# Kernel optimization log

Hardware: AMD Instinct MI355X
Metric: run time of the kernel (lower is better)

## Reference

```python
import jax, jax.numpy as jnp
import numpy as np

B, S, HID, NH, DH = 2, 1024, 4096, 32, 128
ACT_BITS, W_BITS = 8, 4
NEG_INF = float(np.finfo(np.float32).min)


def _qdq(x, bits):
    """Symmetric fake-quant over the last axis (per-token / per-out-channel), with STE."""
    qmax = 2.0 ** (bits - 1) - 1
    s = jnp.maximum(jnp.max(jnp.abs(x), axis=-1, keepdims=True) / qmax, 1e-8)
    q = jnp.clip(jnp.round(x / s), -qmax - 1, qmax) * s
    return x + jax.lax.stop_gradient(q - x)


def _rope_tables(seq_len, dim):
    inv_freq = 1.0 / (10000.0 ** (np.arange(0, dim, 2, dtype=np.float32) / dim))
    t = np.arange(seq_len, dtype=np.float32)
    freqs = np.outer(t, inv_freq)              # [S, DH/2]
    emb = np.concatenate([freqs, freqs], -1)   # [S, DH]
    return jnp.asarray(np.cos(emb)), jnp.asarray(np.sin(emb))


def _rotate_half(x):
    h = x.shape[-1] // 2
    return jnp.concatenate([-x[..., h:], x[..., :h]], axis=-1)


def _norm(x):
    return jnp.linalg.norm(x, axis=-1, keepdims=True)


def setup_inputs() -> dict:
    key = jax.random.key(0)
    ks = jax.random.split(key, 5)
    causal = jnp.where(jnp.tril(jnp.ones((S, S), dtype=bool)), 0.0, NEG_INF).astype(jnp.float32)
    return {
        "hidden_states": jax.random.normal(ks[0], (B, S, HID), jnp.float32),
        "wq": jax.random.normal(ks[1], (HID, HID), jnp.float32) * 0.02,
        "wk": jax.random.normal(ks[2], (HID, HID), jnp.float32) * 0.02,
        "wv": jax.random.normal(ks[3], (HID, HID), jnp.float32) * 0.02,
        "wo": jax.random.normal(ks[4], (HID, HID), jnp.float32) * 0.02,
        "attention_mask": jnp.broadcast_to(causal[None, None], (B, 1, S, S)),
    }


def reference(hidden_states, wq, wk, wv, wo, attention_mask):
    cos, sin = _rope_tables(S, DH)
    cos, sin = cos[None, None], sin[None, None]          # [1,1,S,DH]
    x = _qdq(hidden_states, ACT_BITS)                    # act fake-quant (per token)

    def proj(w):
        return jnp.einsum('bsh,dh->bsd', x, _qdq(w, W_BITS)).reshape(B, S, NH, DH).transpose(0, 2, 1, 3)

    q, k, v = proj(wq), proj(wk), proj(wv)               # [B,H,S,D]
    q = q * cos + _rotate_half(q) * sin
    k = k * cos + _rotate_half(k) * sin

    # qkt_matmul: quant Q and K, rescale scores by quantization norm ratios a1, a2
    x1len = _norm(q)
    qq = _qdq(q, ACT_BITS)
    a1 = _norm(qq) / x1len                               # [B,H,S,1]
    x2len = _norm(k)
    kq = _qdq(k, ACT_BITS)
    a2 = jnp.swapaxes(_norm(kq) / x2len, 2, 3)           # [B,H,1,S]

    attn = jnp.einsum('bhqd,bhkd->bhqk', qq, kq) / np.float32(np.sqrt(DH))
    attn = attn / a1 / a2
    attn = attn + attention_mask
    attn = jnp.maximum(attn, NEG_INF)
    p = jax.nn.softmax(attn.astype(jnp.float32), axis=-1)

    # pv_matmul: quant P and V, rescale output by V's norm ratio
    pq = _qdq(p, ACT_BITS)
    x2len_v = _norm(v)
    vq = _qdq(v, ACT_BITS)
    a2v = _norm(vq) / x2len_v                            # [B,H,S,1]

    out = jnp.einsum('bhqk,bhkd->bhqd', pq, vq) / a2v    # [B,H,S,D]
    out = out.transpose(0, 2, 1, 3).reshape(B, S, HID)
    out = jnp.einsum('bsh,dh->bsd', _qdq(out, ACT_BITS), _qdq(wo, W_BITS))
    return out
```

## Files before the change

kernel.cpp:

```cpp
#include <hip/hip_runtime.h>
#include <hip/hip_bf16.h>
#include <math.h>
#include <stdint.h>

#define NEG_INF_F (-3.4028234663852886e38f)

typedef __bf16 bf16_t;
typedef __bf16 bf16x8 __attribute__((ext_vector_type(8)));
typedef float f32x4 __attribute__((ext_vector_type(4)));
typedef float f32x16 __attribute__((ext_vector_type(16)));
typedef int i32x4 __attribute__((ext_vector_type(4)));
typedef int i32x16 __attribute__((ext_vector_type(16)));
typedef int8_t c8x4 __attribute__((ext_vector_type(4)));

static constexpr int Bb = 2, Ss = 1024, Hid = 4096, Nh = 32, Dh = 128;
static constexpr int Mr = Bb * Ss;
static constexpr int Bh = Bb * Nh;

__device__ __forceinline__ void gload_lds16(const void* g, void* l) {
  __builtin_amdgcn_global_load_lds((const __attribute__((address_space(1))) void*)g,
                                   (__attribute__((address_space(3))) void*)l, 16, 0, 0);
}

__device__ __forceinline__ float wred_max(float v) {
#pragma unroll
  for (int off = 32; off > 0; off >>= 1) v = fmaxf(v, __shfl_xor(v, off));
  return v;
}

__device__ __forceinline__ unsigned pkbf(float a, float b) {
  unsigned short ua = __builtin_bit_cast(unsigned short, (bf16_t)a);
  unsigned short ub = __builtin_bit_cast(unsigned short, (bf16_t)b);
  return (unsigned)ua | ((unsigned)ub << 16);
}

__global__ void rope_table_kernel(float* __restrict__ ctab, float* __restrict__ stab) {
  int i = blockIdx.x * 256 + threadIdx.x;
  int srow = i >> 6, d = i & 63;
  float invf = (float)pow(10000.0, -((double)(2 * d) / (double)Dh));
  float ang = (float)srow * invf;
  ctab[i] = (float)cos((double)ang);
  stab[i] = (float)sin((double)ang);
}

__device__ __forceinline__ void quant_row_body(
    const float* __restrict__ x, int8_t* __restrict__ o, float* __restrict__ scale,
    int row, int ncols, float qmax, float clo, float chi)
{
  const int tid = threadIdx.x;
  const float4* x4 = (const float4*)x;
  const int n4 = ncols >> 2;
  float m = 0.f;
  for (int i = tid; i < n4; i += 256) {
    float4 v = x4[i];
    m = fmaxf(m, fmaxf(fmaxf(fabsf(v.x), fabsf(v.y)), fmaxf(fabsf(v.z), fabsf(v.w))));
  }
  m = wred_max(m);
  __shared__ float red[4];
  if ((tid & 63) == 0) red[tid >> 6] = m;
  __syncthreads();
  m = fmaxf(fmaxf(red[0], red[1]), fmaxf(red[2], red[3]));
  const float s = fmaxf(m / qmax, 1e-8f);
  if (tid == 0) scale[row] = s;
  c8x4* o4 = (c8x4*)o;
  for (int i = tid; i < n4; i += 256) {
    float4 v = x4[i];
    c8x4 r;
    r[0] = (int8_t)(int)fminf(fmaxf(rintf(v.x / s), clo), chi);
    r[1] = (int8_t)(int)fminf(fmaxf(rintf(v.y / s), clo), chi);
    r[2] = (int8_t)(int)fminf(fmaxf(rintf(v.z / s), clo), chi);
    r[3] = (int8_t)(int)fminf(fmaxf(rintf(v.w / s), clo), chi);
    o4[i] = r;
  }
}

__global__ __launch_bounds__(256) void quant_rows_kernel(
    const float* __restrict__ in, int8_t* __restrict__ outq,
    float* __restrict__ scale, int ncols, float qmax, float clo, float chi)
{
  const int row = blockIdx.x;
  quant_row_body(in + (size_t)row * ncols, outq + (size_t)row * ncols, scale,
                 row, ncols, qmax, clo, chi);
}

__global__ __launch_bounds__(256) void quant_w4_kernel(
    const float* __restrict__ w0, const float* __restrict__ w1,
    const float* __restrict__ w2, const float* __restrict__ w3,
    int8_t* __restrict__ o0, int8_t* __restrict__ o1,
    int8_t* __restrict__ o2, int8_t* __restrict__ o3,
    float* __restrict__ s0, float* __restrict__ s1,
    float* __restrict__ s2, float* __restrict__ s3)
{
  const int sel = blockIdx.x >> 12, row = blockIdx.x & 4095;
  const float* in = sel == 0 ? w0 : (sel == 1 ? w1 : (sel == 2 ? w2 : w3));
  int8_t* o = sel == 0 ? o0 : (sel == 1 ? o1 : (sel == 2 ? o2 : o3));
  float* sc = sel == 0 ? s0 : (sel == 1 ? s1 : (sel == 2 ? s2 : s3));
  quant_row_body(in + (size_t)row * Hid, o + (size_t)row * Hid, sc, row, Hid,
                 7.f, -8.f, 7.f);
}

#define GEMM_WAITBAR(N)                                                               \
  asm volatile("s_waitcnt vmcnt(" #N ")" ::: "memory");                               \
  __builtin_amdgcn_sched_barrier(0);                                                  \
  __builtin_amdgcn_s_barrier();                                                       \
  __builtin_amdgcn_sched_barrier(0);

#define GEMM_BARONLY                                                                  \
  __builtin_amdgcn_sched_barrier(0);                                                  \
  __builtin_amdgcn_s_barrier();                                                       \
  __builtin_amdgcn_sched_barrier(0);

#define GEMM_STAGE128(koff, Abuf, Bbuf)                                               \
  _Pragma("unroll")                                                                   \
  for (int r = 0; r < 4; ++r) {                                                       \
    gload_lds16(gA + (koff) + (size_t)r * 32 * K, (Abuf) + r * 4096 + wid * 1024);    \
    gload_lds16(gB + (koff) + (size_t)r * 32 * K, (Bbuf) + r * 4096 + wid * 1024);    \
  }

#define GEMM_PHASE128(Abuf, Bbuf)                                                     \
  _Pragma("unroll")                                                                   \
  for (int g = 0; g < 2; ++g) {                                                       \
    i32x4 af[4], bw[4];                                                               \
    _Pragma("unroll")                                                                 \
    for (int f = 0; f < 4; ++f) {                                                     \
      const int ca = (((g << 2) | kg4) ^ (l15 & 7)) * 16;                             \
      af[f] = *(const i32x4*)&(Abuf)[(wm * 64 + f * 16 + l15) * 128 + ca];            \
      bw[f] = *(const i32x4*)&(Bbuf)[(f * 32 + wn * 16 + l15) * 128 + ca];            \
    }                                                                                 \
    _Pragma("unroll")                                                                 \
    for (int fm = 0; fm < 4; ++fm)                                                    \
      _Pragma("unroll")                                                               \
      for (int fn = 0; fn < 4; ++fn)                                                  \
        acc[fm][fn] = __builtin_amdgcn_mfma_i32_16x16x64_i8(af[fm], bw[fn],           \
                                                            acc[fm][fn], 0, 0, 0);   \
  }

#define GEMM_CORE_PIPE(SMEM)                                                          \
  int8_t* A0 = (int8_t*)(SMEM);                                                       \
  int8_t* A1 = (int8_t*)(SMEM) + 16384;                                               \
  int8_t* B0 = (int8_t*)(SMEM) + 32768;                                               \
  int8_t* B1 = (int8_t*)(SMEM) + 49152;                                               \
  const int strow = wid * 8 + (lane >> 3);                                            \
  const int schunk = ((lane & 7) ^ (lane >> 3)) * 16;                                 \
  const int8_t* gA = A + (size_t)(bm + strow) * K + schunk;                           \
  const int8_t* gB = W + (size_t)(bn + strow) * K + schunk;                           \
  i32x4 acc[4][4] = {};                                                               \
  GEMM_STAGE128(0, A0, B0)                                                            \
  GEMM_STAGE128(128, A1, B1)                                                          \
  for (int k0 = 0; k0 + 512 <= K; k0 += 256) {                                        \
    GEMM_WAITBAR(8)                                                                   \
    GEMM_PHASE128(A0, B0)                                                             \
    GEMM_BARONLY                                                                      \
    GEMM_STAGE128(k0 + 256, A0, B0)                                                   \
    GEMM_WAITBAR(8)                                                                   \
    GEMM_PHASE128(A1, B1)                                                             \
    GEMM_BARONLY                                                                      \
    GEMM_STAGE128(k0 + 384, A1, B1)                                                   \
  }                                                                                   \
  GEMM_WAITBAR(8)                                                                     \
  GEMM_PHASE128(A0, B0)                                                               \
  GEMM_BARONLY                                                                        \
  GEMM_WAITBAR(0)                                                                     \
  GEMM_PHASE128(A1, B1)

__global__ __launch_bounds__(256) void qkv_gemm_kernel(
    const int8_t* __restrict__ A, const float* __restrict__ sA,
    const int8_t* __restrict__ wqz, const int8_t* __restrict__ wkz, const int8_t* __restrict__ wvz,
    const float* __restrict__ swq, const float* __restrict__ swk, const float* __restrict__ swv,
    int8_t* __restrict__ qqb, float* __restrict__ Fq,
    int8_t* __restrict__ kqb, float* __restrict__ Fk,
    bf16_t* __restrict__ vdq, float* __restrict__ a2vp,
    const float* __restrict__ ctab, const float* __restrict__ stab)
{
  __shared__ __align__(16) char smem[65536 + 3072];
  float (*s_red)[128][3] = (float (*)[128][3])(smem + 65536);

  const int tid = threadIdx.x, lane = tid & 63, wid = tid >> 6;
  const int id = blockIdx.x;
  const int xcd = id & 7, within = id >> 3;
  const int nIdx = xcd * 12 + (within >> 4);
  const int mIdx = within & 15;
  const int wsel = nIdx >> 5, head = nIdx & 31;
  const int bm = mIdx * 128, bn = head * 128;
  const int8_t* W = wsel == 0 ? wqz : (wsel == 1 ? wkz : wvz);
  const float* sW = wsel == 0 ? swq : (wsel == 1 ? swk : swv);
  constexpr int K = Hid;

  const int wm = wid >> 1, wn = wid & 1;
  const int l15 = lane & 15, kg4 = lane >> 4;

  GEMM_CORE_PIPE(smem)

  float sav[4][4], swv_[4];
#pragma unroll
  for (int fm = 0; fm < 4; ++fm)
#pragma unroll
    for (int j = 0; j < 4; ++j) sav[fm][j] = sA[bm + wm * 64 + fm * 16 + kg4 * 4 + j];
#pragma unroll
  for (int fn = 0; fn < 4; ++fn) swv_[fn] = sW[bn + fn * 32 + wn * 16 + l15];

  float val[4][4][4];
#pragma unroll
  for (int fm = 0; fm < 4; ++fm)
#pragma unroll
    for (int fn = 0; fn < 4; ++fn)
#pragma unroll
      for (int j = 0; j < 4; ++j)
        val[fm][fn][j] = (float)acc[fm][fn][j] * sav[fm][j] * swv_[fn];

  const int b = bm >> 10;
  const int bh = b * Nh + head;
  float r_[4][4][4];
  if (wsel != 2) {
    const int dmA = wn * 16 + l15, dmB = 32 + wn * 16 + l15;
#pragma unroll
    for (int fm = 0; fm < 4; ++fm)
#pragma unroll
      for (int j = 0; j < 4; ++j) {
        const int srow = (bm + wm * 64 + fm * 16 + kg4 * 4 + j) & (Ss - 1);
        const float cA = ctab[srow * 64 + dmA], cB = ctab[srow * 64 + dmB];
        const float sA_ = stab[srow * 64 + dmA], sB_ = stab[srow * 64 + dmB];
        r_[fm][0][j] = __fsub_rn(__fmul_rn(val[fm][0][j], cA), __fmul_rn(val[fm][2][j], sA_));
        r_[fm][1][j] = __fsub_rn(__fmul_rn(val[fm][1][j], cB), __fmul_rn(val[fm][3][j], sB_));
        r_[fm][2][j] = __fadd_rn(__fmul_rn(val[fm][2][j], cA), __fmul_rn(val[fm][0][j], sA_));
        r_[fm][3][j] = __fadd_rn(__fmul_rn(val[fm][3][j], cB), __fmul_rn(val[fm][1][j], sB_));
      }
  } else {
#pragma unroll
    for (int fm = 0; fm < 4; ++fm)
#pragma unroll
      for (int fn = 0; fn < 4; ++fn)
#pragma unroll
        for (int j = 0; j < 4; ++j) r_[fm][fn][j] = val[fm][fn][j];
  }
  float ma_[4][4], n2_[4][4];
#pragma unroll
  for (int fm = 0; fm < 4; ++fm)
#pragma unroll
    for (int j = 0; j < 4; ++j) {
      float ma = 0.f, n2 = 0.f;
#pragma unroll
      for (int fn = 0; fn < 4; ++fn) {
        const float x = r_[fm][fn][j];
        ma = fmaxf(ma, fabsf(x));
        n2 += x * x;
      }
#pragma unroll
      for (int off = 1; off < 16; off <<= 1) {
        ma = fmaxf(ma, __shfl_xor(ma, off));
        n2 += __shfl_xor(n2, off);
      }
      ma_[fm][j] = ma;
      n2_[fm][j] = n2;
    }
  if (l15 == 0) {
#pragma unroll
    for (int fm = 0; fm < 4; ++fm)
#pragma unroll
      for (int j = 0; j < 4; ++j) {
        const int rl = wm * 64 + fm * 16 + kg4 * 4 + j;
        s_red[wn][rl][0] = ma_[fm][j];
        s_red[wn][rl][1] = n2_[fm][j];
      }
  }
  __syncthreads();
  float qc[4][4][4], svl[4][4], n2c[4][4], nq2_[4][4];
#pragma unroll
  for (int fm = 0; fm < 4; ++fm)
#pragma unroll
    for (int j = 0; j < 4; ++j) {
      const int rl = wm * 64 + fm * 16 + kg4 * 4 + j;
      const float ma = fmaxf(ma_[fm][j], s_red[wn ^ 1][rl][0]);
      const float n2 = n2_[fm][j] + s_red[wn ^ 1][rl][1];
      const float s = fmaxf(ma / 127.0f, 1e-8f);
      float nq2 = 0.f;
#pragma unroll
      for (int fn = 0; fn < 4; ++fn) {
        const float q = fminf(fmaxf(rintf(r_[fm][fn][j] / s), -128.f), 127.f);
        qc[fm][fn][j] = q;
        nq2 += q * q;
      }
#pragma unroll
      for (int off = 1; off < 16; off <<= 1) nq2 += __shfl_xor(nq2, off);
      svl[fm][j] = s;
      n2c[fm][j] = n2;
      nq2_[fm][j] = nq2;
    }
  __syncthreads();
  if (l15 == 0) {
#pragma unroll
    for (int fm = 0; fm < 4; ++fm)
#pragma unroll
      for (int j = 0; j < 4; ++j)
        s_red[wn][wm * 64 + fm * 16 + kg4 * 4 + j][2] = nq2_[fm][j];
  }
  __syncthreads();

  if (wsel != 2) {
    int8_t* outq = (wsel == 0) ? qqb : kqb;
    float* Ff = (wsel == 0) ? Fq : Fk;
#pragma unroll
    for (int fm = 0; fm < 4; ++fm)
#pragma unroll
      for (int j = 0; j < 4; ++j) {
        const int rl = wm * 64 + fm * 16 + kg4 * 4 + j;
        const int stok = (bm + rl) & (Ss - 1);
        const size_t rowBase = ((size_t)bh * Ss + stok) * Dh;
#pragma unroll
        for (int fn = 0; fn < 4; ++fn)
          outq[rowBase + fn * 32 + wn * 16 + l15] = (int8_t)(int)qc[fm][fn][j];
        if (wn == 0 && l15 == 0) {
          const float nq2 = nq2_[fm][j] + s_red[1][rl][2];
          Ff[(size_t)bh * Ss + stok] = sqrtf(n2c[fm][j] / nq2) * 0.2973017787506803f;
        }
      }
  } else {
    bf16_t* svt = (bf16_t*)smem;
#pragma unroll
    for (int fm = 0; fm < 4; ++fm)
#pragma unroll
      for (int j = 0; j < 4; ++j) {
        const int t = wm * 64 + fm * 16 + kg4 * 4 + j;
#pragma unroll
        for (int fn = 0; fn < 4; ++fn) {
          const int d = fn * 32 + wn * 16 + l15;
          svt[d * 136 + t] = (bf16_t)(qc[fm][fn][j] * svl[fm][j]);
        }
        if (wn == 0 && l15 == 0) {
          const float nq2 = nq2_[fm][j] + s_red[1][t][2];
          a2vp[(size_t)bh * Ss + ((bm + t) & (Ss - 1))] =
              svl[fm][j] * sqrtf(nq2) / sqrtf(n2c[fm][j]);
        }
      }
    __syncthreads();
    const int d = tid >> 1, toff = (tid & 1) * 64;
    const int s0 = bm & (Ss - 1);
    const bf16_t* src = svt + d * 136 + toff;
    bf16_t* dst = vdq + ((size_t)bh * Dh + d) * Ss + s0 + toff;
#pragma unroll
    for (int k = 0; k < 8; ++k) {
      bf16x8 tv;
#pragma unroll
      for (int e = 0; e < 8; ++e) tv[e] = src[k * 8 + e];
      *(bf16x8*)(dst + k * 8) = tv;
    }
  }
}

__global__ __launch_bounds__(256) void gemm0_kernel(
    const int8_t* __restrict__ A, const float* __restrict__ sA,
    const int8_t* __restrict__ W, const float* __restrict__ sW,
    float* __restrict__ out, int M, int N, int K)
{
  __shared__ __align__(16) int8_t As[128 * 128];
  __shared__ __align__(16) int8_t Bs[128 * 128];
  const int tid = threadIdx.x, lane = tid & 63, wid = tid >> 6;
  const int id = blockIdx.x;
  const int xcd = id & 7, within = id >> 3;
  const int nIdx = xcd * 4 + (within >> 4);
  const int mIdx = within & 15;
  const int bm = mIdx * 128, bn = nIdx * 128;
  const int wm = wid >> 1, wn = wid & 1;
  const int l15 = lane & 15, kg4 = lane >> 4;

  const int strow = wid * 8 + (lane >> 3);
  const int schunk = ((lane & 7) ^ (lane >> 3)) * 16;
  const int8_t* gA = A + (size_t)(bm + strow) * K + schunk;
  const int8_t* gB = W + (size_t)(bn + strow) * K + schunk;

  i32x4 acc[4][4] = {};
  for (int k0 = 0; k0 < K; k0 += 128) {
    if (k0) __syncthreads();
#pragma unroll
    for (int r = 0; r < 4; ++r) {
      gload_lds16(gA + k0 + (size_t)r * 32 * K, As + r * 4096 + wid * 1024);
      gload_lds16(gB + k0 + (size_t)r * 32 * K, Bs + r * 4096 + wid * 1024);
    }
    __syncthreads();
#pragma unroll
    for (int g = 0; g < 2; ++g) {
      i32x4 af[4], bw[4];
#pragma unroll
      for (int f = 0; f < 4; ++f) {
        const int ca = (((g << 2) | kg4) ^ (l15 & 7)) * 16;
        af[f] = *(const i32x4*)&As[(wm * 64 + f * 16 + l15) * 128 + ca];
        bw[f] = *(const i32x4*)&Bs[(f * 32 + wn * 16 + l15) * 128 + ca];
      }
#pragma unroll
      for (int fm = 0; fm < 4; ++fm)
#pragma unroll
        for (int fn = 0; fn < 4; ++fn)
          acc[fm][fn] = __builtin_amdgcn_mfma_i32_16x16x64_i8(af[fm], bw[fn], acc[fm][fn], 0, 0, 0);
    }
  }
#pragma unroll
  for (int fm = 0; fm < 4; ++fm) {
#pragma unroll
    for (int j = 0; j < 4; ++j) {
      const int row = bm + wm * 64 + fm * 16 + kg4 * 4 + j;
      const float sa = sA[row];
#pragma unroll
      for (int fn = 0; fn < 4; ++fn) {
        const int col = bn + fn * 32 + wn * 16 + l15;
        out[(size_t)row * N + col] = (float)acc[fm][fn][j] * sa * sW[col];
      }
    }
  }
}

#define KR(r) (((r) & 3) + 8 * ((r) >> 2) + 4 * hi)
__global__ __launch_bounds__(64, 2) void attn_kernel(
    const int8_t* __restrict__ qq, const int8_t* __restrict__ kq,
    const bf16_t* __restrict__ vdqt,
    const float* __restrict__ Fq, const float* __restrict__ Fk,
    const float* __restrict__ A2v, float* __restrict__ oattn)
{
  const int bh = blockIdx.x, b = bh >> 5, h = bh & 31;
  const int lane = threadIdx.x & 63;
  const int l31 = lane & 31, hi = lane >> 5;
  const int u = 31 - (int)blockIdx.y;
  const int q0 = u * 32;
  const int nt = u + 1;
  const size_t bhS = (size_t)bh * Ss;

  const int8_t* qrow = qq + (bhS + q0 + l31) * Dh + hi * 16;
  i32x4 qf[4];
#pragma unroll
  for (int c = 0; c < 4; ++c) qf[c] = *(const i32x4*)(qrow + c * 32);
  const float fq = Fq[bhS + q0 + l31];
  const int qcol = q0 + l31;

  float m = NEG_INF_F;
  int t = 0;
  for (; t + 1 < nt; t += 2) {
    const int kb0 = t * 32, kb1 = kb0 + 32;
    const int8_t* kr0 = kq + (bhS + kb0 + l31) * Dh + hi * 16;
    const int8_t* kr1 = kq + (bhS + kb1 + l31) * Dh + hi * 16;
    i32x16 ca = {}, cb = {}, da = {}, db = {};
    ca = __builtin_amdgcn_mfma_i32_32x32x32_i8(*(const i32x4*)(kr0),      qf[0], ca, 0, 0, 0);
    cb = __builtin_amdgcn_mfma_i32_32x32x32_i8(*(const i32x4*)(kr0 + 64), qf[2], cb, 0, 0, 0);
    da = __builtin_amdgcn_mfma_i32_32x32x32_i8(*(const i32x4*)(kr1),      qf[0], da, 0, 0, 0);
    db = __builtin_amdgcn_mfma_i32_32x32x32_i8(*(const i32x4*)(kr1 + 64), qf[2], db, 0, 0, 0);
    ca = __builtin_amdgcn_mfma_i32_32x32x32_i8(*(const i32x4*)(kr0 + 32), qf[1], ca, 0, 0, 0);
    cb = __builtin_amdgcn_mfma_i32_32x32x32_i8(*(const i32x4*)(kr0 + 96), qf[3], cb, 0, 0, 0);
    da = __builtin_amdgcn_mfma_i32_32x32x32_i8(*(const i32x4*)(kr1 + 32), qf[1], da, 0, 0, 0);
    db = __builtin_amdgcn_mfma_i32_32x32x32_i8(*(const i32x4*)(kr1 + 96), qf[3], db, 0, 0, 0);
    float4 fk40[4], fk41[4];
#pragma unroll
    for (int g = 0; g < 4; ++g) fk40[g] = *(const float4*)&Fk[bhS + kb0 + g * 8 + 4 * hi];
#pragma unroll
    for (int g = 0; g < 4; ++g) fk41[g] = *(const float4*)&Fk[bhS + kb1 + g * 8 + 4 * hi];
    const bool diag1 = (t + 1 == nt - 1);
#pragma unroll
    for (int r = 0; r < 16; ++r) {
      m = fmaxf(m, (float)(ca[r] + cb[r]) * fq * ((const float*)&fk40[r >> 2])[r & 3]);
      const float v1 = (float)(da[r] + db[r]) * fq * ((const float*)&fk41[r >> 2])[r & 3];
      if (!diag1 || (kb1 + KR(r) <= qcol)) m = fmaxf(m, v1);
    }
  }
  if (t < nt) {
    const int kb = t * 32;
    const int8_t* krow = kq + (bhS + kb + l31) * Dh + hi * 16;
    i32x16 ca = {}, cb = {};
    ca = __builtin_amdgcn_mfma_i32_32x32x32_i8(*(const i32x4*)(krow),      qf[0], ca, 0, 0, 0);
    cb = __builtin_amdgcn_mfma_i32_32x32x32_i8(*(const i32x4*)(krow + 64), qf[2], cb, 0, 0, 0);
    ca = __builtin_amdgcn_mfma_i32_32x32x32_i8(*(const i32x4*)(krow + 32), qf[1], ca, 0, 0, 0);
    cb = __builtin_amdgcn_mfma_i32_32x32x32_i8(*(const i32x4*)(krow + 96), qf[3], cb, 0, 0, 0);
    float4 fk4[4];
#pragma unroll
    for (int g = 0; g < 4; ++g) fk4[g] = *(const float4*)&Fk[bhS + kb + g * 8 + 4 * hi];
#pragma unroll
    for (int r = 0; r < 16; ++r) {
      const float v = (float)(ca[r] + cb[r]) * fq * ((const float*)&fk4[r >> 2])[r & 3];
      if (kb + KR(r) <= qcol) m = fmaxf(m, v);
    }
  }
  m = fmaxf(m, __shfl_xor(m, 32));

  float z = 0.f;
  f32x16 oacc[4] = {};
  for (int tt = 0; tt < nt; ++tt) {
    const int kb = tt * 32;
    const int8_t* krow = kq + (bhS + kb + l31) * Dh + hi * 16;
    i32x16 ca = {}, cb = {};
    ca = __builtin_amdgcn_mfma_i32_32x32x32_i8(*(const i32x4*)(krow),      qf[0], ca, 0, 0, 0);
    cb = __builtin_amdgcn_mfma_i32_32x32x32_i8(*(const i32x4*)(krow + 64), qf[2], cb, 0, 0, 0);
    ca = __builtin_amdgcn_mfma_i32_32x32x32_i8(*(const i32x4*)(krow + 32), qf[1], ca, 0, 0, 0);
    cb = __builtin_amdgcn_mfma_i32_32x32x32_i8(*(const i32x4*)(krow + 96), qf[3], cb, 0, 0, 0);
    float4 fk4[4];
#pragma unroll
    for (int g = 0; g < 4; ++g) fk4[g] = *(const float4*)&Fk[bhS + kb + g * 8 + 4 * hi];
    float p[16];
    const bool diag = (tt == nt - 1);
#pragma unroll
    for (int r = 0; r < 16; ++r) {
      float v = (float)(ca[r] + cb[r]) * fq * ((const float*)&fk4[r >> 2])[r & 3];
      if (diag && (kb + KR(r) > qcol)) v = NEG_INF_F;
      const float e = __expf(v - m);
      z += e;
      p[r] = rintf(127.0f * e);
    }
#pragma unroll
    for (int s = 0; s < 2; ++s) {
      const int rs = s * 8;
      unsigned k0 = pkbf(p[rs + 0], p[rs + 1]);
      unsigned k1 = pkbf(p[rs + 2], p[rs + 3]);
      unsigned k2 = pkbf(p[rs + 4], p[rs + 5]);
      unsigned k3 = pkbf(p[rs + 6], p[rs + 7]);
      unsigned sx0 = __shfl_xor(k0, 32);
      unsigned sx1 = __shfl_xor(k1, 32);
      unsigned sx2 = __shfl_xor(k2, 32);
      unsigned sx3 = __shfl_xor(k3, 32);
      uint4 ww;
      ww.x = hi ? sx2 : k0;
      ww.y = hi ? sx3 : k1;
      ww.z = hi ? k2 : sx0;
      ww.w = hi ? k3 : sx1;
      const bf16x8 af = __builtin_bit_cast(bf16x8, ww);
      const int kg2 = kb + s * 16 + hi * 8;
#pragma unroll
      for (int dt = 0; dt < 4; ++dt) {
        const bf16x8 vf = *(const bf16x8*)(vdqt + ((size_t)bh * Dh + dt * 32 + l31) * Ss + kg2);
        oacc[dt] = __builtin_amdgcn_mfma_f32_32x32x16_bf16(af, vf, oacc[dt], 0, 0, 0);
      }
    }
  }
  z += __shfl_xor(z, 32);
  const float osc = (1.0f / z) / 127.0f / A2v[bhS + q0 + l31];
#pragma unroll
  for (int dt = 0; dt < 4; ++dt) {
#pragma unroll
    for (int r = 0; r < 16; ++r) {
      const int q = q0 + KR(r);
      const float oscr = __shfl(osc, KR(r));
      oattn[((size_t)b * Ss + q) * Hid + h * Dh + dt * 32 + l31] = oacc[dt][r] * oscr;
    }
  }
}

extern "C" void kernel_launch(void* const* d_in, const int* in_sizes, int n_in,
                              void* d_out, int out_size, void* d_ws, size_t ws_size,
                              hipStream_t stream)
{
  const float* hidden = (const float*)d_in[0];
  const float* wq = (const float*)d_in[1];
  const float* wk = (const float*)d_in[2];
  const float* wv = (const float*)d_in[3];
  const float* wo = (const float*)d_in[4];
  float* out = (float*)d_out;

  char* p = (char*)d_ws;
  auto alloc = [&](size_t bytes) -> char* {
    char* r = p; p += (bytes + 255) & ~(size_t)255; return r;
  };
  int8_t* xq   = (int8_t*)alloc((size_t)Mr * Hid);
  int8_t* wb0  = (int8_t*)alloc((size_t)Hid * Hid);
  int8_t* wb1  = (int8_t*)alloc((size_t)Hid * Hid);
  int8_t* wb2  = (int8_t*)alloc((size_t)Hid * Hid);
  int8_t* wb3  = (int8_t*)alloc((size_t)Hid * Hid);
  float*  oat  = (float*) alloc((size_t)Bh * Ss * Dh * sizeof(float));
  int8_t* qqb  = (int8_t*)alloc((size_t)Bh * Ss * Dh);
  int8_t* kqb  = (int8_t*)alloc((size_t)Bh * Ss * Dh);
  bf16_t* vdqt = (bf16_t*)alloc((size_t)Bh * Dh * Ss * sizeof(bf16_t));
  float* sxa = (float*)alloc((size_t)Mr * sizeof(float));
  float* sw0 = (float*)alloc((size_t)Hid * sizeof(float));
  float* sw1 = (float*)alloc((size_t)Hid * sizeof(float));
  float* sw2 = (float*)alloc((size_t)Hid * sizeof(float));
  float* sw3 = (float*)alloc((size_t)Hid * sizeof(float));
  float* Fq  = (float*)alloc((size_t)Bh * Ss * sizeof(float));
  float* Fk  = (float*)alloc((size_t)Bh * Ss * sizeof(float));
  float* A2v = (float*)alloc((size_t)Bh * Ss * sizeof(float));
  float* soa = (float*)alloc((size_t)Mr * sizeof(float));
  float* ctab = (float*)alloc((size_t)Ss * 64 * sizeof(float));
  float* stab = (float*)alloc((size_t)Ss * 64 * sizeof(float));
  int8_t* oq  = xq;

  rope_table_kernel<<<Ss * 64 / 256, 256, 0, stream>>>(ctab, stab);
  quant_rows_kernel<<<Mr, 256, 0, stream>>>(hidden, xq, sxa, Hid, 127.f, -128.f, 127.f);
  quant_w4_kernel<<<4 * Hid, 256, 0, stream>>>(wq, wk, wv, wo, wb0, wb1, wb2, wb3,
                                               sw0, sw1, sw2, sw3);

  qkv_gemm_kernel<<<1536, 256, 0, stream>>>(xq, sxa, wb0, wb1, wb2, sw0, sw1, sw2,
                                            qqb, Fq, kqb, Fk, vdqt, A2v, ctab, stab);

  dim3 ga(Bh, 32);
  attn_kernel<<<ga, 64, 0, stream>>>(qqb, kqb, vdqt, Fq, Fk, A2v, oat);

  quant_rows_kernel<<<Mr, 256, 0, stream>>>(oat, oq, soa, Hid, 127.f, -128.f, 127.f);
  gemm0_kernel<<<512, 256, 0, stream>>>(oq, soa, wb3, sw3, out, Mr, Hid, Hid);
}
```

Before: 373.1 us.

## Enlarge QKV GEMM tile to 256x128 with 64-wide K stages

The fused QKV int8 GEMM now computes 256x128 output tiles per block (8x4 MFMA fragments per wave) using K-steps of 64 instead of 128, halving the grid to 768 blocks. Each B fragment is reused across more A rows, which cuts global and LDS traffic per MFMA and shrinks the shared-memory footprint to 48KB by reusing staging buffers for the reduction and transpose scratch. The epilogue is reworked to store V's transposed tile in two halves and to reuse one register array in place. The trade is higher register pressure (128 accumulator registers), which may lower occupancy, plus fewer blocks to spread across the CUs.

```diff
diff --git a/kernel.cpp b/kernel.cpp
--- a/kernel.cpp
+++ b/kernel.cpp
@@ -99,69 +99,40 @@
                  7.f, -8.f, 7.f);
 }
 
-#define GEMM_WAITBAR(N)                                                               \
+#define QKV_WAITBAR(N)                                                                \
   asm volatile("s_waitcnt vmcnt(" #N ")" ::: "memory");                               \
   __builtin_amdgcn_sched_barrier(0);                                                  \
   __builtin_amdgcn_s_barrier();                                                       \
   __builtin_amdgcn_sched_barrier(0);
 
-#define GEMM_BARONLY                                                                  \
+#define QKV_BARONLY                                                                   \
   __builtin_amdgcn_sched_barrier(0);                                                  \
   __builtin_amdgcn_s_barrier();                                                       \
   __builtin_amdgcn_sched_barrier(0);
 
-#define GEMM_STAGE128(koff, Abuf, Bbuf)                                               \
+#define QKV_STAGE(koff, Abuf, Bbuf)                                                   \
   _Pragma("unroll")                                                                   \
-  for (int r = 0; r < 4; ++r) {                                                       \
-    gload_lds16(gA + (koff) + (size_t)r * 32 * K, (Abuf) + r * 4096 + wid * 1024);    \
-    gload_lds16(gB + (koff) + (size_t)r * 32 * K, (Bbuf) + r * 4096 + wid * 1024);    \
-  }
-
-#define GEMM_PHASE128(Abuf, Bbuf)                                                     \
+  for (int r = 0; r < 4; ++r)                                                         \
+    gload_lds16(gA + (koff) + (size_t)r * 64 * K, (Abuf) + r * 4096 + wid * 1024);    \
   _Pragma("unroll")                                                                   \
-  for (int g = 0; g < 2; ++g) {                                                       \
-    i32x4 af[4], bw[4];                                                               \
+  for (int r = 0; r < 2; ++r)                                                         \
+    gload_lds16(gB + (koff) + (size_t)r * 64 * K, (Bbuf) + r * 4096 + wid * 1024);
+
+#define QKV_PHASE(Abuf, Bbuf)                                                         \
+  {                                                                                   \
+    i32x4 bw[4];                                                                      \
     _Pragma("unroll")                                                                 \
-    for (int f = 0; f < 4; ++f) {                                                     \
-      const int ca = (((g << 2) | kg4) ^ (l15 & 7)) * 16;                             \
-      af[f] = *(const i32x4*)&(Abuf)[(wm * 64 + f * 16 + l15) * 128 + ca];            \
-      bw[f] = *(const i32x4*)&(Bbuf)[(f * 32 + wn * 16 + l15) * 128 + ca];            \
-    }                                                                                 \
+    for (int f = 0; f < 4; ++f)                                                       \
+      bw[f] = *(const i32x4*)&(Bbuf)[(f * 32 + wn * 16 + l15) * 64 + ck];             \
     _Pragma("unroll")                                                                 \
-    for (int fm = 0; fm < 4; ++fm)                                                    \
+    for (int fm = 0; fm < 8; ++fm) {                                                  \
+      i32x4 af = *(const i32x4*)&(Abuf)[(wm * 128 + fm * 16 + l15) * 64 + ck];        \
       _Pragma("unroll")                                                               \
       for (int fn = 0; fn < 4; ++fn)                                                  \
-        acc[fm][fn] = __builtin_amdgcn_mfma_i32_16x16x64_i8(af[fm], bw[fn],           \
+        acc[fm][fn] = __builtin_amdgcn_mfma_i32_16x16x64_i8(af, bw[fn],               \
                                                             acc[fm][fn], 0, 0, 0);   \
-  }
-
-#define GEMM_CORE_PIPE(SMEM)                                                          \
-  int8_t* A0 = (int8_t*)(SMEM);                                                       \
-  int8_t* A1 = (int8_t*)(SMEM) + 16384;                                               \
-  int8_t* B0 = (int8_t*)(SMEM) + 32768;                                               \
-  int8_t* B1 = (int8_t*)(SMEM) + 49152;                                               \
-  const int strow = wid * 8 + (lane >> 3);                                            \
-  const int schunk = ((lane & 7) ^ (lane >> 3)) * 16;                                 \
-  const int8_t* gA = A + (size_t)(bm + strow) * K + schunk;                           \
-  const int8_t* gB = W + (size_t)(bn + strow) * K + schunk;                           \
-  i32x4 acc[4][4] = {};                                                               \
-  GEMM_STAGE128(0, A0, B0)                                                            \
-  GEMM_STAGE128(128, A1, B1)                                                          \
-  for (int k0 = 0; k0 + 512 <= K; k0 += 256) {                                        \
-    GEMM_WAITBAR(8)                                                                   \
-    GEMM_PHASE128(A0, B0)                                                             \
-    GEMM_BARONLY                                                                      \
-    GEMM_STAGE128(k0 + 256, A0, B0)                                                   \
-    GEMM_WAITBAR(8)                                                                   \
-    GEMM_PHASE128(A1, B1)                                                             \
-    GEMM_BARONLY                                                                      \
-    GEMM_STAGE128(k0 + 384, A1, B1)                                                   \
-  }                                                                                   \
-  GEMM_WAITBAR(8)                                                                     \
-  GEMM_PHASE128(A0, B0)                                                               \
-  GEMM_BARONLY                                                                        \
-  GEMM_WAITBAR(0)                                                                     \
-  GEMM_PHASE128(A1, B1)
+    }                                                                                 \
+  }
 
 __global__ __launch_bounds__(256) void qkv_gemm_kernel(
     const int8_t* __restrict__ A, const float* __restrict__ sA,
@@ -172,76 +143,98 @@
     bf16_t* __restrict__ vdq, float* __restrict__ a2vp,
     const float* __restrict__ ctab, const float* __restrict__ stab)
 {
-  __shared__ __align__(16) char smem[65536 + 3072];
-  float (*s_red)[128][3] = (float (*)[128][3])(smem + 65536);
+  __shared__ __align__(16) char smem[49152];
+  int8_t* A0 = (int8_t*)smem;
+  int8_t* B0 = (int8_t*)smem + 16384;
+  int8_t* A1 = (int8_t*)smem + 24576;
+  int8_t* B1 = (int8_t*)smem + 40960;
+  float (*s_red)[256][3] = (float (*)[256][3])smem;
+  bf16_t* svt = (bf16_t*)(smem + 8192);
 
   const int tid = threadIdx.x, lane = tid & 63, wid = tid >> 6;
   const int id = blockIdx.x;
   const int xcd = id & 7, within = id >> 3;
-  const int nIdx = xcd * 12 + (within >> 4);
-  const int mIdx = within & 15;
+  const int nIdx = xcd * 12 + (within >> 3);
+  const int mIdx = within & 7;
   const int wsel = nIdx >> 5, head = nIdx & 31;
-  const int bm = mIdx * 128, bn = head * 128;
+  const int bm = mIdx * 256, bn = head * 128;
   const int8_t* W = wsel == 0 ? wqz : (wsel == 1 ? wkz : wvz);
   const float* sW = wsel == 0 ? swq : (wsel == 1 ? swk : swv);
   constexpr int K = Hid;
 
   const int wm = wid >> 1, wn = wid & 1;
   const int l15 = lane & 15, kg4 = lane >> 4;
-
-  GEMM_CORE_PIPE(smem)
-
-  float sav[4][4], swv_[4];
-#pragma unroll
-  for (int fm = 0; fm < 4; ++fm)
-#pragma unroll
-    for (int j = 0; j < 4; ++j) sav[fm][j] = sA[bm + wm * 64 + fm * 16 + kg4 * 4 + j];
+  const int ck = (kg4 ^ ((l15 >> 1) & 3)) * 16;
+
+  const int strow = tid >> 2;
+  const int schunk = ((tid & 3) ^ ((tid >> 3) & 3)) * 16;
+  const int8_t* gA = A + (size_t)(bm + strow) * K + schunk;
+  const int8_t* gB = W + (size_t)(bn + strow) * K + schunk;
+
+  i32x4 acc[8][4] = {};
+  QKV_STAGE(0, A0, B0)
+  QKV_STAGE(64, A1, B1)
+  for (int k0 = 0; k0 + 256 <= K; k0 += 128) {
+    QKV_WAITBAR(6)
+    QKV_PHASE(A0, B0)
+    QKV_BARONLY
+    QKV_STAGE(k0 + 128, A0, B0)
+    QKV_WAITBAR(6)
+    QKV_PHASE(A1, B1)
+    QKV_BARONLY
+    QKV_STAGE(k0 + 192, A1, B1)
+  }
+  QKV_WAITBAR(6)
+  QKV_PHASE(A0, B0)
+  QKV_BARONLY
+  QKV_WAITBAR(0)
+  QKV_PHASE(A1, B1)
+
+  float sav[8][4], swv_[4];
+#pragma unroll
+  for (int fm = 0; fm < 8; ++fm)
+#pragma unroll
+    for (int j = 0; j < 4; ++j) sav[fm][j] = sA[bm + wm * 128 + fm * 16 + kg4 * 4 + j];
 #pragma unroll
   for (int fn = 0; fn < 4; ++fn) swv_[fn] = sW[bn + fn * 32 + wn * 16 + l15];
 
-  float val[4][4][4];
-#pragma unroll
-  for (int fm = 0; fm < 4; ++fm)
+  float w[8][4][4];
+#pragma unroll
+  for (int fm = 0; fm < 8; ++fm)
 #pragma unroll
     for (int fn = 0; fn < 4; ++fn)
 #pragma unroll
       for (int j = 0; j < 4; ++j)
-        val[fm][fn][j] = (float)acc[fm][fn][j] * sav[fm][j] * swv_[fn];
+        w[fm][fn][j] = (float)acc[fm][fn][j] * sav[fm][j] * swv_[fn];
 
   const int b = bm >> 10;
   const int bh = b * Nh + head;
-  float r_[4][4][4];
   if (wsel != 2) {
     const int dmA = wn * 16 + l15, dmB = 32 + wn * 16 + l15;
 #pragma unroll
-    for (int fm = 0; fm < 4; ++fm)
+    for (int fm = 0; fm < 8; ++fm)
 #pragma unroll
       for (int j = 0; j < 4; ++j) {
-        const int srow = (bm + wm * 64 + fm * 16 + kg4 * 4 + j) & (Ss - 1);
+        const int srow = (bm + wm * 128 + fm * 16 + kg4 * 4 + j) & (Ss - 1);
         const float cA = ctab[srow * 64 + dmA], cB = ctab[srow * 64 + dmB];
         const float sA_ = stab[srow * 64 + dmA], sB_ = stab[srow * 64 + dmB];
-        r_[fm][0][j] = __fsub_rn(__fmul_rn(val[fm][0][j], cA), __fmul_rn(val[fm][2][j], sA_));
-        r_[fm][1][j] = __fsub_rn(__fmul_rn(val[fm][1][j], cB), __fmul_rn(val[fm][3][j], sB_));
-        r_[fm][2][j] = __fadd_rn(__fmul_rn(val[fm][2][j], cA), __fmul_rn(val[fm][0][j], sA_));
-        r_[fm][3][j] = __fadd_rn(__fmul_rn(val[fm][3][j], cB), __fmul_rn(val[fm][1][j], sB_));
-      }
-  } else {
-#pragma unroll
-    for (int fm = 0; fm < 4; ++fm)
-#pragma unroll
-      for (int fn = 0; fn < 4; ++fn)
-#pragma unroll
-        for (int j = 0; j < 4; ++j) r_[fm][fn][j] = val[fm][fn][j];
-  }
-  float ma_[4][4], n2_[4][4];
-#pragma unroll
-  for (int fm = 0; fm < 4; ++fm)
+        const float a0 = w[fm][0][j], a1 = w[fm][1][j];
+        const float a2 = w[fm][2][j], a3 = w[fm][3][j];
+        w[fm][0][j] = __fsub_rn(__fmul_rn(a0, cA), __fmul_rn(a2, sA_));
+        w[fm][1][j] = __fsub_rn(__fmul_rn(a1, cB), __fmul_rn(a3, sB_));
+        w[fm][2][j] = __fadd_rn(__fmul_rn(a2, cA), __fmul_rn(a0, sA_));
+        w[fm][3][j] = __fadd_rn(__fmul_rn(a3, cB), __fmul_rn(a1, sB_));
+      }
+  }
+  float ma_[8][4], n2_[8][4];
+#pragma unroll
+  for (int fm = 0; fm < 8; ++fm)
 #pragma unroll
     for (int j = 0; j < 4; ++j) {
       float ma = 0.f, n2 = 0.f;
 #pragma unroll
       for (int fn = 0; fn < 4; ++fn) {
-        const float x = r_[fm][fn][j];
+        const float x = w[fm][fn][j];
         ma = fmaxf(ma, fabsf(x));
         n2 += x * x;
       }
@@ -255,29 +248,29 @@
     }
   if (l15 == 0) {
 #pragma unroll
-    for (int fm = 0; fm < 4; ++fm)
+    for (int fm = 0; fm < 8; ++fm)
 #pragma unroll
       for (int j = 0; j < 4; ++j) {
-        const int rl = wm * 64 + fm * 16 + kg4 * 4 + j;
+        const int rl = wm * 128 + fm * 16 + kg4 * 4 + j;
         s_red[wn][rl][0] = ma_[fm][j];
         s_red[wn][rl][1] = n2_[fm][j];
       }
   }
   __syncthreads();
-  float qc[4][4][4], svl[4][4], n2c[4][4], nq2_[4][4];
-#pragma unroll
-  for (int fm = 0; fm < 4; ++fm)
+  float svl[8][4], n2c[8][4], nq2_[8][4];
+#pragma unroll
+  for (int fm = 0; fm < 8; ++fm)
 #pragma unroll
     for (int j = 0; j < 4; ++j) {
-      const int rl = wm * 64 + fm * 16 + kg4 * 4 + j;
+      const int rl = wm * 128 + fm * 16 + kg4 * 4 + j;
       const float ma = fmaxf(ma_[fm][j], s_red[wn ^ 1][rl][0]);
       const float n2 = n2_[fm][j] + s_red[wn ^ 1][rl][1];
       const float s = fmaxf(ma / 127.0f, 1e-8f);
       float nq2 = 0.f;
 #pragma unroll
       for (int fn = 0; fn < 4; ++fn) {
-        const float q = fminf(fmaxf(rintf(r_[fm][fn][j] / s), -128.f), 127.f);
-        qc[fm][fn][j] = q;
+        const float q = fminf(fmaxf(rintf(w[fm][fn][j] / s), -128.f), 127.f);
+        w[fm][fn][j] = q;
         nq2 += q * q;
       }
 #pragma unroll
@@ -289,10 +282,10 @@
   __syncthreads();
   if (l15 == 0) {
 #pragma unroll
-    for (int fm = 0; fm < 4; ++fm)
+    for (int fm = 0; fm < 8; ++fm)
 #pragma unroll
       for (int j = 0; j < 4; ++j)
-        s_red[wn][wm * 64 + fm * 16 + kg4 * 4 + j][2] = nq2_[fm][j];
+        s_red[wn][wm * 128 + fm * 16 + kg4 * 4 + j][2] = nq2_[fm][j];
   }
   __syncthreads();
 
@@ -300,49 +293,59 @@
     int8_t* outq = (wsel == 0) ? qqb : kqb;
     float* Ff = (wsel == 0) ? Fq : Fk;
 #pragma unroll
-    for (int fm = 0; fm < 4; ++fm)
+    for (int fm = 0; fm < 8; ++fm)
 #pragma unroll
       for (int j = 0; j < 4; ++j) {
-        const int rl = wm * 64 + fm * 16 + kg4 * 4 + j;
+        const int rl = wm * 128 + fm * 16 + kg4 * 4 + j;
         const int stok = (bm + rl) & (Ss - 1);
         const size_t rowBase = ((size_t)bh * Ss + stok) * Dh;
 #pragma unroll
         for (int fn = 0; fn < 4; ++fn)
-          outq[rowBase + fn * 32 + wn * 16 + l15] = (int8_t)(int)qc[fm][fn][j];
+          outq[rowBase + fn * 32 + wn * 16 + l15] = (int8_t)(int)w[fm][fn][j];
         if (wn == 0 && l15 == 0) {
           const float nq2 = nq2_[fm][j] + s_red[1][rl][2];
           Ff[(size_t)bh * Ss + stok] = sqrtf(n2c[fm][j] / nq2) * 0.2973017787506803f;
         }
       }
   } else {
-    bf16_t* svt = (bf16_t*)smem;
-#pragma unroll
-    for (int fm = 0; fm < 4; ++fm)
-#pragma unroll
-      for (int j = 0; j < 4; ++j) {
-        const int t = wm * 64 + fm * 16 + kg4 * 4 + j;
-#pragma unroll
-        for (int fn = 0; fn < 4; ++fn) {
-          const int d = fn * 32 + wn * 16 + l15;
-          svt[d * 136 + t] = (bf16_t)(qc[fm][fn][j] * svl[fm][j]);
-        }
-        if (wn == 0 && l15 == 0) {
-          const float nq2 = nq2_[fm][j] + s_red[1][t][2];
-          a2vp[(size_t)bh * Ss + ((bm + t) & (Ss - 1))] =
+    if (wn == 0 && l15 == 0) {
+#pragma unroll
+      for (int fm = 0; fm < 8; ++fm)
+#pragma unroll
+        for (int j = 0; j < 4; ++j) {
+          const int rl = wm * 128 + fm * 16 + kg4 * 4 + j;
+          const float nq2 = nq2_[fm][j] + s_red[1][rl][2];
+          a2vp[(size_t)bh * Ss + ((bm + rl) & (Ss - 1))] =
               svl[fm][j] * sqrtf(nq2) / sqrtf(n2c[fm][j]);
         }
-      }
-    __syncthreads();
-    const int d = tid >> 1, toff = (tid & 1) * 64;
-    const int s0 = bm & (Ss - 1);
-    const bf16_t* src = svt + d * 136 + toff;
-    bf16_t* dst = vdq + ((size_t)bh * Dh + d) * Ss + s0 + toff;
-#pragma unroll
-    for (int k = 0; k < 8; ++k) {
-      bf16x8 tv;
-#pragma unroll
-      for (int e = 0; e < 8; ++e) tv[e] = src[k * 8 + e];
-      *(bf16x8*)(dst + k * 8) = tv;
+    }
+    for (int half = 0; half < 2; ++half) {
+      if (wm == half) {
+#pragma unroll
+        for (int fm = 0; fm < 8; ++fm)
+#pragma unroll
+          for (int j = 0; j < 4; ++j) {
+            const int t = fm * 16 + kg4 * 4 + j;
+#pragma unroll
+            for (int fn = 0; fn < 4; ++fn) {
+              const int d = fn * 32 + wn * 16 + l15;
+              svt[d * 136 + t] = (bf16_t)(w[fm][fn][j] * svl[fm][j]);
+            }
+          }
+      }
+      __syncthreads();
+      const int d = tid >> 1, toff = (tid & 1) * 64;
+      const int s0h = (bm & (Ss - 1)) + half * 128;
+      const bf16_t* src = svt + d * 136 + toff;
+      bf16_t* dst = vdq + ((size_t)bh * Dh + d) * Ss + s0h + toff;
+#pragma unroll
+      for (int k = 0; k < 8; ++k) {
+        bf16x8 tv;
+#pragma unroll
+        for (int e = 0; e < 8; ++e) tv[e] = src[k * 8 + e];
+        *(bf16x8*)(dst + k * 8) = tv;
+      }
+      __syncthreads();
     }
   }
 }
@@ -580,8 +583,8 @@
   quant_w4_kernel<<<4 * Hid, 256, 0, stream>>>(wq, wk, wv, wo, wb0, wb1, wb2, wb3,
                                                sw0, sw1, sw2, sw3);
 
-  qkv_gemm_kernel<<<1536, 256, 0, stream>>>(xq, sxa, wb0, wb1, wb2, sw0, sw1, sw2,
-                                            qqb, Fq, kqb, Fk, vdqt, A2v, ctab, stab);
+  qkv_gemm_kernel<<<768, 256, 0, stream>>>(xq, sxa, wb0, wb1, wb2, sw0, sw1, sw2,
+                                           qqb, Fq, kqb, Fk, vdqt, A2v, ctab, stab);
 
   dim3 ga(Bh, 32);
   attn_kernel<<<ga, 64, 0, stream>>>(qqb, kqb, vdqt, Fq, Fk, A2v, oat);
```

Measured after the change: 507.1 us. 35.9% more time.
